# Performance work log

Measured on AMD Instinct MI355X. Metric: run time of the kernel, lower is better.

## Reference

```python
import jax, jax.numpy as jnp
import numpy as np

NUM_HEADS = 32
ROPE_BASE = 10000.0
VISION_TOKEN_TYPE = 1


def _rotate_half(x):
    x1, x2 = jnp.split(x, 2, axis=-1)
    return jnp.concatenate([-x2, x1], axis=-1)


def _rope_cos_sin(position_ids, head_dim, dtype):
    # position_ids: [L] int -> cos/sin [L, head_dim]
    inv_freq = 1.0 / (ROPE_BASE ** (jnp.arange(0, head_dim, 2, dtype=jnp.float32) / head_dim))
    freqs = position_ids.astype(jnp.float32)[:, None] * inv_freq[None, :]  # [L, head_dim//2]
    emb = jnp.concatenate([freqs, freqs], axis=-1)  # [L, head_dim]
    return jnp.cos(emb).astype(dtype), jnp.sin(emb).astype(dtype)


def setup_inputs() -> dict:
    key = jax.random.key(0)
    ks = jax.random.split(key, 7)
    B, L, D = 2, 1024, 4096
    w_scale = 0.02
    return {
        'hidden_states': jax.random.normal(ks[0], (B, L, D), dtype=jnp.float32),
        'token_type_ids': jax.random.randint(ks[1], (B, L), 0, 2, dtype=jnp.int32),
        'position_ids': jnp.arange(L, dtype=jnp.int64),
        'w_qkv_vis': jax.random.normal(ks[2], (D, 3 * D), dtype=jnp.float32) * w_scale,
        'w_qkv_lang': jax.random.normal(ks[3], (D, 3 * D), dtype=jnp.float32) * w_scale,
        'w_dense_vis': jax.random.normal(ks[4], (D, D), dtype=jnp.float32) * w_scale,
        'w_dense_lang': jax.random.normal(ks[5], (D, D), dtype=jnp.float32) * w_scale,
    }


def reference(hidden_states, token_type_ids, position_ids, w_qkv_vis, w_qkv_lang, w_dense_vis, w_dense_lang):
    B, L, D = hidden_states.shape
    H = NUM_HEADS
    Dh = D // H

    # expert masks: a token is 'vision' iff it and the NEXT token are vision type
    tt = token_type_ids
    vmask = jnp.zeros(tt.shape, dtype=bool)
    vmask = vmask.at[:, :-1].set((tt[:, :-1] == VISION_TOKEN_TYPE) & (tt[:, 1:] == VISION_TOKEN_TYPE))  # [B, L]

    # dual-expert fused QKV projection (mask-select between experts)
    qkv = jnp.where(vmask[..., None],
                    hidden_states @ w_qkv_vis,
                    hidden_states @ w_qkv_lang)  # [B, L, 3D]
    q, k, v = jnp.split(qkv, 3, axis=-1)
    q = q.reshape(B, L, H, Dh)
    k = k.reshape(B, L, H, Dh)
    v = v.reshape(B, L, H, Dh)

    # rotary embedding
    cos, sin = _rope_cos_sin(position_ids, Dh, q.dtype)  # [L, Dh]
    cos = cos[None, :, None, :]
    sin = sin[None, :, None, :]
    q = q * cos + _rotate_half(q) * sin
    k = k * cos + _rotate_half(k) * sin

    # causal self-attention (prefill semantics of paged_attention_fwd)
    scale = 1.0 / jnp.sqrt(jnp.asarray(Dh, dtype=q.dtype))
    scores = jnp.einsum('blhd,bmhd->bhlm', q, k) * scale  # [B, H, L, L]
    causal = jnp.tril(jnp.ones((L, L), dtype=bool))
    scores = jnp.where(causal[None, None], scores, jnp.asarray(-1e30, dtype=scores.dtype))
    probs = jax.nn.softmax(scores, axis=-1)
    ctx = jnp.einsum('bhlm,bmhd->blhd', probs, v).reshape(B, L, D)

    # dual-expert output projection
    attn_output = jnp.where(vmask[..., None],
                            ctx @ w_dense_vis,
                            ctx @ w_dense_lang)  # [B, L, D]
    return attn_output
```

## Files before the change

### kernel.cpp

```cpp
#include <hip/hip_runtime.h>
#include <math.h>

typedef unsigned short u16;
typedef __attribute__((ext_vector_type(4))) float f32x4;
typedef __attribute__((ext_vector_type(8))) __bf16 bf16x8;
typedef __attribute__((ext_vector_type(8))) u16 u16x8;
typedef __attribute__((ext_vector_type(4))) u16 u16x4;

#define D_MODEL 4096
#define NQKV    12288
#define BL      2048
#define L_SEQ   1024
#define NH      32
#define DH      128

__device__ __forceinline__ u16 f2bf(float f) {
    union { float f; unsigned u; } v; v.f = f;
    unsigned r = (v.u + 0x7fffu + ((v.u >> 16) & 1u)) >> 16;
    return (u16)r;
}
__device__ __forceinline__ float bf2f(u16 b) {
    union { unsigned u; float f; } v; v.u = ((unsigned)b) << 16;
    return v.f;
}
__device__ __forceinline__ void gload_lds16(const void* g, void* l) {
    __builtin_amdgcn_global_load_lds((const __attribute__((address_space(1))) void*)g,
                                     (__attribute__((address_space(3))) void*)l, 16, 0, 0);
}
__device__ __forceinline__ f32x4 mfma_bf16(bf16x8 a, bf16x8 b, f32x4 c) {
    return __builtin_amdgcn_mfma_f32_16x16x32_bf16(a, b, c, 0, 0, 0);
}

#define BAR()      asm volatile("s_barrier" ::: "memory")
#define WAIT_VM4() asm volatile("s_waitcnt vmcnt(4)" ::: "memory")
#define WAIT_VM0() asm volatile("s_waitcnt vmcnt(0)" ::: "memory")

__global__ __launch_bounds__(256) void convert_f32_bf16(const float* __restrict__ in,
                                                        u16* __restrict__ out, int n4) {
    int i = blockIdx.x * 256 + threadIdx.x;
    if (i < n4) {
        float4 v = ((const float4*)in)[i];
        u16x4 o;
        o[0] = f2bf(v.x); o[1] = f2bf(v.y); o[2] = f2bf(v.z); o[3] = f2bf(v.w);
        ((u16x4*)out)[i] = o;
    }
}

__global__ __launch_bounds__(256) void transpose_convert(const float* __restrict__ W,
                                                         u16* __restrict__ Wt, int K, int N) {
    __shared__ float t[32][33];
    int tx = threadIdx.x, ty = threadIdx.y;
    int nt = blockIdx.x * 32, kt = blockIdx.y * 32;
#pragma unroll
    for (int i = 0; i < 4; ++i)
        t[ty + i * 8][tx] = W[(size_t)(kt + ty + i * 8) * N + nt + tx];
    __syncthreads();
#pragma unroll
    for (int i = 0; i < 4; ++i)
        Wt[(size_t)(nt + ty + i * 8) * K + kt + tx] = f2bf(t[tx][ty + i * 8]);
}

__global__ __launch_bounds__(256) void mask_scan(const int* __restrict__ tt,
                                                 int* __restrict__ lists,
                                                 int* __restrict__ counts) {
    __shared__ int buf[256];
    int tid = threadIdx.x;
    int base = tid * 8;
    int flags = 0, cv = 0;
#pragma unroll
    for (int j = 0; j < 8; ++j) {
        int i = base + j;
        int l = i & (L_SEQ - 1);
        int f = (l < L_SEQ - 1) && (tt[i] == 1) && (tt[i + 1] == 1);
        flags |= f << j; cv += f;
    }
    buf[tid] = cv; __syncthreads();
    for (int d = 1; d < 256; d <<= 1) {
        int t = (tid >= d) ? buf[tid - d] : 0;
        __syncthreads();
        buf[tid] += t;
        __syncthreads();
    }
    int vs = buf[tid] - cv;
    int ls = base - vs;
    int total_v = buf[255];
#pragma unroll
    for (int j = 0; j < 8; ++j) {
        int i = base + j;
        if ((flags >> j) & 1) lists[vs++] = i;
        else                  lists[2048 + ls++] = i;
    }
    if (tid == 0) { counts[0] = total_v; counts[1] = 2048 - total_v; }
}

template <typename OutT>
__global__ __launch_bounds__(512, 2) void gemm_expert(
    const u16* __restrict__ A, const u16* __restrict__ BtVis, const u16* __restrict__ BtLang,
    OutT* __restrict__ C, const int* __restrict__ lists, const int* __restrict__ counts, int ldc) {
    const int e = blockIdx.z;
    const int cnt = counts[e];
    const int m0 = blockIdx.y * 256;
    if (m0 >= cnt) return;
    const u16* Bt = (e == 0) ? BtVis : BtLang;
    const int* list = lists + e * 2048;
    const int n0 = blockIdx.x * 256;
    const int tid = threadIdx.x, lane = tid & 63, w = tid >> 6;
    const int wm = w >> 2, wn = w & 3;
    const int l16 = lane & 15, quad = lane >> 4;

    __shared__ __align__(16) u16 lds[2][2][2][8192];

    const int r0 = tid >> 2;
    const int cs = (tid & 3) ^ ((r0 >> 1) & 3);
    const char* pa0 = (const char*)(A + (size_t)list[min(m0 + r0, cnt - 1)] * D_MODEL) + cs * 16;
    const char* pa1 = (const char*)(A + (size_t)list[min(m0 + 128 + r0, cnt - 1)] * D_MODEL) + cs * 16;
    const char* pb0 = (const char*)(Bt + (size_t)(n0 + r0) * D_MODEL) + cs * 16;
    const char* pb1 = (const char*)(Bt + (size_t)(n0 + 128 + r0) * D_MODEL) + cs * 16;
    const int dst0 = w * 512;
    const int dst1 = 4096 + w * 512;

    auto STAGE = [&](int buf, int mat, int kh, int tk) {
        const int kbyte = tk * 128 + kh * 64;
        const char* g0 = (mat == 0) ? pa0 : pb0;
        const char* g1 = (mat == 0) ? pa1 : pb1;
        u16* d = &lds[buf][mat][kh][0];
        gload_lds16(g0 + kbyte, d + dst0);
        gload_lds16(g1 + kbyte, d + dst1);
    };

    f32x4 acc[8][4] = {};
    const int NT = D_MODEL / 64;

    STAGE(0, 0, 0, 0); STAGE(0, 1, 0, 0); STAGE(0, 0, 1, 0); STAGE(0, 1, 1, 0);
    WAIT_VM4();
    BAR();

    for (int t = 0; t < NT; ++t) {
        const int c = t & 1, nb = c ^ 1;
        const bool pf = (t + 1 < NT);
        bf16x8 af[4], bf[4];

#pragma unroll
        for (int ni = 0; ni < 4; ++ni) {
            int row = wn * 64 + ni * 16 + l16;
            bf[ni] = *(const bf16x8*)&lds[c][1][0][row * 32 + (quad ^ ((row >> 1) & 3)) * 8];
        }
#pragma unroll
        for (int mi = 0; mi < 4; ++mi) {
            int row = wm * 128 + mi * 16 + l16;
            af[mi] = *(const bf16x8*)&lds[c][0][0][row * 32 + (quad ^ ((row >> 1) & 3)) * 8];
        }
        if (pf) STAGE(nb, 0, 0, t + 1);
        BAR();
        __builtin_amdgcn_s_setprio(1);
#pragma unroll
        for (int mi = 0; mi < 4; ++mi)
#pragma unroll
            for (int ni = 0; ni < 4; ++ni)
                acc[mi][ni] = mfma_bf16(af[mi], bf[ni], acc[mi][ni]);
        __builtin_amdgcn_s_setprio(0);
        BAR();

#pragma unroll
        for (int mi = 0; mi < 4; ++mi) {
            int row = wm * 128 + 64 + mi * 16 + l16;
            af[mi] = *(const bf16x8*)&lds[c][0][0][row * 32 + (quad ^ ((row >> 1) & 3)) * 8];
        }
        if (pf) STAGE(nb, 1, 0, t + 1);
        BAR();
        __builtin_amdgcn_s_setprio(1);
#pragma unroll
        for (int mi = 0; mi < 4; ++mi)
#pragma unroll
            for (int ni = 0; ni < 4; ++ni)
                acc[4 + mi][ni] = mfma_bf16(af[mi], bf[ni], acc[4 + mi][ni]);
        __builtin_amdgcn_s_setprio(0);
        if (pf) WAIT_VM4(); else WAIT_VM0();
        BAR();

#pragma unroll
        for (int ni = 0; ni < 4; ++ni) {
            int row = wn * 64 + ni * 16 + l16;
            bf[ni] = *(const bf16x8*)&lds[c][1][1][row * 32 + (quad ^ ((row >> 1) & 3)) * 8];
        }
#pragma unroll
        for (int mi = 0; mi < 4; ++mi) {
            int row = wm * 128 + mi * 16 + l16;
            af[mi] = *(const bf16x8*)&lds[c][0][1][row * 32 + (quad ^ ((row >> 1) & 3)) * 8];
        }
        if (pf) STAGE(nb, 0, 1, t + 1);
        BAR();
        __builtin_amdgcn_s_setprio(1);
#pragma unroll
        for (int mi = 0; mi < 4; ++mi)
#pragma unroll
            for (int ni = 0; ni < 4; ++ni)
                acc[mi][ni] = mfma_bf16(af[mi], bf[ni], acc[mi][ni]);
        __builtin_amdgcn_s_setprio(0);
        BAR();

#pragma unroll
        for (int mi = 0; mi < 4; ++mi) {
            int row = wm * 128 + 64 + mi * 16 + l16;
            af[mi] = *(const bf16x8*)&lds[c][0][1][row * 32 + (quad ^ ((row >> 1) & 3)) * 8];
        }
        if (pf) STAGE(nb, 1, 1, t + 1);
        BAR();
        __builtin_amdgcn_s_setprio(1);
#pragma unroll
        for (int mi = 0; mi < 4; ++mi)
#pragma unroll
            for (int ni = 0; ni < 4; ++ni)
                acc[4 + mi][ni] = mfma_bf16(af[mi], bf[ni], acc[4 + mi][ni]);
        __builtin_amdgcn_s_setprio(0);
        if (pf) WAIT_VM4();
        BAR();
    }

#pragma unroll
    for (int mf = 0; mf < 8; ++mf) {
#pragma unroll
        for (int r = 0; r < 4; ++r) {
            int slot = m0 + wm * 128 + mf * 16 + quad * 4 + r;
            if (slot < cnt) {
                int row = list[slot];
                size_t rb = (size_t)row * ldc + n0 + wn * 64 + l16;
#pragma unroll
                for (int ni = 0; ni < 4; ++ni) {
                    float v = acc[mf][ni][r];
                    if constexpr (sizeof(OutT) == 2) C[rb + ni * 16] = (OutT)f2bf(v);
                    else                             C[rb + ni * 16] = v;
                }
            }
        }
    }
}

__global__ __launch_bounds__(256) void rope_kernel(u16* __restrict__ qkv,
                                                   const int* __restrict__ posi) {
    int idx = blockIdx.x * 256 + threadIdx.x;
    int t = idx >> 11;
    int rem = idx & 2047;
    int h = rem >> 6;
    int j = rem & 63;
    int l = t & (L_SEQ - 1);
    int is_i32 = posi[1];
    int pv = is_i32 ? posi[l] : posi[2 * l];
    float p = (float)pv;
    float inv = expf(-(float)j * 0.14391156831212787f);
    float ang = p * inv;
    float s, c;
    sincosf(ang, &s, &c);
    size_t base = (size_t)t * NQKV + h * DH + j;
    float x1 = bf2f(qkv[base]), x2 = bf2f(qkv[base + 64]);
    qkv[base]      = f2bf(x1 * c - x2 * s);
    qkv[base + 64] = f2bf(x2 * c + x1 * s);
    size_t kb = base + D_MODEL;
    x1 = bf2f(qkv[kb]); x2 = bf2f(qkv[kb + 64]);
    qkv[kb]      = f2bf(x1 * c - x2 * s);
    qkv[kb + 64] = f2bf(x2 * c + x1 * s);
}

__global__ __launch_bounds__(256, 2) void attn_kernel(const u16* __restrict__ qkv,
                                                      u16* __restrict__ ctx) {
    const int qt = (int)gridDim.x - 1 - (int)blockIdx.x;
    const int h = blockIdx.y, b = blockIdx.z;
    const int tid = threadIdx.x, lane = tid & 63, w = tid >> 6;
    const int quad = lane >> 4, l16 = lane & 15;

    __shared__ __align__(16) u16 Ks[2][64 * 128];
    __shared__ __align__(16) u16 Vt[2][128 * 64];
    __shared__ __align__(16) u16 Ps[4][16 * 64];

    const size_t qbase = ((size_t)(b * L_SEQ + qt * 64 + w * 16 + l16)) * NQKV + h * DH;
    bf16x8 aq[4];
#pragma unroll
    for (int kc = 0; kc < 4; ++kc)
        aq[kc] = *(const bf16x8*)&qkv[qbase + kc * 32 + quad * 8];

    int srow[4], schk[4];
#pragma unroll
    for (int i = 0; i < 4; ++i) {
        int idx = i * 256 + tid;
        srow[i] = idx >> 4;
        schk[i] = idx & 15;
    }
    const size_t kv0 = ((size_t)(b * L_SEQ)) * NQKV + D_MODEL + h * DH;

    float m_i[4], l_i[4];
    f32x4 o[8] = {};
#pragma unroll
    for (int r = 0; r < 4; ++r) { m_i[r] = -1e30f; l_i[r] = 0.f; }
    const float scale = 0.08838834764831845f;
    const int jmax = qt + 1;

    {
        u16x8 kr[4], vr[4];
#pragma unroll
        for (int i = 0; i < 4; ++i) {
            size_t g = kv0 + (size_t)srow[i] * NQKV + schk[i] * 8;
            kr[i] = *(const u16x8*)&qkv[g];
            vr[i] = *(const u16x8*)&qkv[g + D_MODEL];
        }
#pragma unroll
        for (int i = 0; i < 4; ++i) {
            int r = srow[i], c = schk[i];
            *(u16x8*)&Ks[0][r * 128 + ((c ^ (r & 7)) * 8)] = kr[i];
#pragma unroll
            for (int e = 0; e < 8; ++e) {
                int d = c * 8 + e;
                int sw = (r >> 3) ^ ((d ^ (d >> 3)) & 7);
                Vt[0][d * 64 + sw * 8 + (r & 7)] = vr[i][e];
            }
        }
    }
    __syncthreads();

    for (int jt = 0; jt < jmax; ++jt) {
        const int cur = jt & 1;
        const bool pf = (jt + 1 < jmax);

        u16x8 kr[4], vr[4];
        if (pf) {
            const size_t kb = kv0 + (size_t)((jt + 1) * 64) * NQKV;
#pragma unroll
            for (int i = 0; i < 4; ++i) {
                size_t g = kb + (size_t)srow[i] * NQKV + schk[i] * 8;
                kr[i] = *(const u16x8*)&qkv[g];
                vr[i] = *(const u16x8*)&qkv[g + D_MODEL];
            }
        }

        f32x4 s[4] = {};
        __builtin_amdgcn_s_setprio(1);
#pragma unroll
        for (int sub = 0; sub < 4; ++sub) {
            const int row = sub * 16 + l16;
#pragma unroll
            for (int kc = 0; kc < 4; ++kc) {
                bf16x8 bk = *(const bf16x8*)&Ks[cur][row * 128 + (((kc * 4 + quad) ^ (row & 7)) * 8)];
                s[sub] = mfma_bf16(aq[kc], bk, s[sub]);
            }
        }
        __builtin_amdgcn_s_setprio(0);

        const int qg = qt * 64 + w * 16 + quad * 4;
        float p[4][4], mx[4];
#pragma unroll
        for (int r = 0; r < 4; ++r) mx[r] = -1e30f;
#pragma unroll
        for (int sub = 0; sub < 4; ++sub) {
            const int kg = jt * 64 + sub * 16 + l16;
#pragma unroll
            for (int r = 0; r < 4; ++r) {
                float sv = (kg <= qg + r) ? s[sub][r] * scale : -1e30f;
                p[sub][r] = sv;
                mx[r] = fmaxf(mx[r], sv);
            }
        }
#pragma unroll
        for (int d = 1; d < 16; d <<= 1)
#pragma unroll
            for (int r = 0; r < 4; ++r) mx[r] = fmaxf(mx[r], __shfl_xor(mx[r], d));
        float alpha[4], rs[4];
#pragma unroll
        for (int r = 0; r < 4; ++r) {
            float mn = fmaxf(m_i[r], mx[r]);
            alpha[r] = __expf(m_i[r] - mn);
            m_i[r] = mn;
            rs[r] = 0.f;
        }
#pragma unroll
        for (int sub = 0; sub < 4; ++sub)
#pragma unroll
            for (int r = 0; r < 4; ++r) {
                p[sub][r] = __expf(p[sub][r] - m_i[r]);
                rs[r] += p[sub][r];
            }
#pragma unroll
        for (int d = 1; d < 16; d <<= 1)
#pragma unroll
            for (int r = 0; r < 4; ++r) rs[r] += __shfl_xor(rs[r], d);

#pragma unroll
        for (int sub = 0; sub < 4; ++sub)
#pragma unroll
            for (int r = 0; r < 4; ++r) {
                const int q = quad * 4 + r;
                const int chunk = sub * 2 + (l16 >> 3);
                Ps[w][q * 64 + ((chunk ^ (q & 7)) * 8) + (l16 & 7)] = f2bf(p[sub][r]);
            }
#pragma unroll
        for (int r = 0; r < 4; ++r) l_i[r] = l_i[r] * alpha[r] + rs[r];
#pragma unroll
        for (int n = 0; n < 8; ++n)
#pragma unroll
            for (int r = 0; r < 4; ++r) o[n][r] *= alpha[r];

        __builtin_amdgcn_s_setprio(1);
#pragma unroll
        for (int ks = 0; ks < 2; ++ks) {
            bf16x8 ap = *(const bf16x8*)&Ps[w][l16 * 64 + (((ks * 4 + quad) ^ (l16 & 7)) * 8)];
#pragma unroll
            for (int n = 0; n < 8; ++n) {
                const int d = n * 16 + l16;
                bf16x8 bv = *(const bf16x8*)&Vt[cur][d * 64 + (((ks * 4 + quad) ^ ((d ^ (d >> 3)) & 7)) * 8)];
                o[n] = mfma_bf16(ap, bv, o[n]);
            }
        }
        __builtin_amdgcn_s_setprio(0);

        if (pf) {
            const int nb = cur ^ 1;
#pragma unroll
            for (int i = 0; i < 4; ++i) {
                int r = srow[i], c = schk[i];
                *(u16x8*)&Ks[nb][r * 128 + ((c ^ (r & 7)) * 8)] = kr[i];
#pragma unroll
                for (int e = 0; e < 8; ++e) {
                    int d = c * 8 + e;
                    int sw = (r >> 3) ^ ((d ^ (d >> 3)) & 7);
                    Vt[nb][d * 64 + sw * 8 + (r & 7)] = vr[i][e];
                }
            }
        }
        __syncthreads();
    }

    const int tglob = b * L_SEQ + qt * 64 + w * 16 + quad * 4;
#pragma unroll
    for (int r = 0; r < 4; ++r) {
        float invl = 1.f / l_i[r];
#pragma unroll
        for (int n = 0; n < 8; ++n)
            ctx[(size_t)(tglob + r) * D_MODEL + h * DH + n * 16 + l16] = f2bf(o[n][r] * invl);
    }
}

extern "C" void kernel_launch(void* const* d_in, const int* in_sizes, int n_in,
                              void* d_out, int out_size, void* d_ws, size_t ws_size,
                              hipStream_t stream) {
    const float* hidden = (const float*)d_in[0];
    const int* tt = (const int*)d_in[1];
    const int* pos = (const int*)d_in[2];
    const float* wqv = (const float*)d_in[3];
    const float* wql = (const float*)d_in[4];
    const float* wdv = (const float*)d_in[5];
    const float* wdl = (const float*)d_in[6];
    float* out = (float*)d_out;

    char* ws = (char*)d_ws;
    size_t off = 0;
    auto alloc = [&](size_t bytes) {
        char* p = ws + off;
        off += (bytes + 255) & ~(size_t)255;
        return p;
    };
    u16* WqvT = (u16*)alloc((size_t)NQKV * D_MODEL * 2);
    u16* WqlT = (u16*)alloc((size_t)NQKV * D_MODEL * 2);
    u16* WdvT = (u16*)alloc((size_t)D_MODEL * D_MODEL * 2);
    u16* WdlT = (u16*)alloc((size_t)D_MODEL * D_MODEL * 2);
    u16* Abf  = (u16*)alloc((size_t)BL * D_MODEL * 2);
    u16* QKV  = (u16*)alloc((size_t)BL * NQKV * 2);
    u16* CTX  = (u16*)alloc((size_t)BL * D_MODEL * 2);
    int* lists  = (int*)alloc(4096 * sizeof(int));
    int* counts = (int*)alloc(256);

    convert_f32_bf16<<<BL * D_MODEL / 4 / 256, 256, 0, stream>>>(hidden, Abf, BL * D_MODEL / 4);
    transpose_convert<<<dim3(NQKV / 32, D_MODEL / 32), dim3(32, 8), 0, stream>>>(wqv, WqvT, D_MODEL, NQKV);
    transpose_convert<<<dim3(NQKV / 32, D_MODEL / 32), dim3(32, 8), 0, stream>>>(wql, WqlT, D_MODEL, NQKV);
    transpose_convert<<<dim3(D_MODEL / 32, D_MODEL / 32), dim3(32, 8), 0, stream>>>(wdv, WdvT, D_MODEL, D_MODEL);
    transpose_convert<<<dim3(D_MODEL / 32, D_MODEL / 32), dim3(32, 8), 0, stream>>>(wdl, WdlT, D_MODEL, D_MODEL);
    mask_scan<<<1, 256, 0, stream>>>(tt, lists, counts);
    gemm_expert<u16><<<dim3(NQKV / 256, 8, 2), 512, 0, stream>>>(Abf, WqvT, WqlT, QKV, lists, counts, NQKV);
    rope_kernel<<<BL * NH * 64 / 256, 256, 0, stream>>>(QKV, pos);
    attn_kernel<<<dim3(16, NH, 2), 256, 0, stream>>>(QKV, CTX);
    gemm_expert<float><<<dim3(D_MODEL / 256, 8, 2), 512, 0, stream>>>(CTX, WdvT, WdlT, out, lists, counts, D_MODEL);
}
```

Measured before the change: 1.025 ms.

## Use 5-slot LDS ring in expert GEMM, rewrite weight transpose, fast rope math

The expert GEMM swaps its double-buffered 4-quarter LDS layout for a 5-slot ring. Each quarter-tile load is issued right after the MFMA block that frees a slot, so prefetch runs deeper, and launch bounds rise to 4 blocks per SM. The weight transpose-convert drops the shared-memory tile: each thread now reads 8 strided floats and writes one 16-byte packed bf16 vector. RoPE uses the fast __expf/__sincosf intrinsics. Risks include lower accuracy in RoPE, strided uncoalesced global reads in the transpose, and register pressure from the higher occupancy target with 128 accumulators.

```diff
diff --git a/kernel.cpp b/kernel.cpp
--- a/kernel.cpp
+++ b/kernel.cpp
@@ -48,16 +48,14 @@
 
 __global__ __launch_bounds__(256) void transpose_convert(const float* __restrict__ W,
                                                          u16* __restrict__ Wt, int K, int N) {
-    __shared__ float t[32][33];
-    int tx = threadIdx.x, ty = threadIdx.y;
-    int nt = blockIdx.x * 32, kt = blockIdx.y * 32;
-#pragma unroll
-    for (int i = 0; i < 4; ++i)
-        t[ty + i * 8][tx] = W[(size_t)(kt + ty + i * 8) * N + nt + tx];
-    __syncthreads();
-#pragma unroll
-    for (int i = 0; i < 4; ++i)
-        Wt[(size_t)(nt + ty + i * 8) * K + kt + tx] = f2bf(t[tx][ty + i * 8]);
+    const int l = threadIdx.x & 63, w = threadIdx.x >> 6;
+    const int nt = blockIdx.x * 64, kt = blockIdx.y * 32 + w * 8;
+    const int n = nt + l;
+    u16x8 o;
+#pragma unroll
+    for (int j = 0; j < 8; ++j)
+        o[j] = f2bf(W[(size_t)(kt + j) * N + n]);
+    *(u16x8*)&Wt[(size_t)n * K + kt] = o;
 }
 
 __global__ __launch_bounds__(256) void mask_scan(const int* __restrict__ tt,
@@ -94,7 +92,7 @@
 }
 
 template <typename OutT>
-__global__ __launch_bounds__(512, 2) void gemm_expert(
+__global__ __launch_bounds__(512, 4) void gemm_expert(
     const u16* __restrict__ A, const u16* __restrict__ BtVis, const u16* __restrict__ BtLang,
     OutT* __restrict__ C, const int* __restrict__ lists, const int* __restrict__ counts, int ldc) {
     const int e = blockIdx.z;
@@ -108,7 +106,7 @@
     const int wm = w >> 2, wn = w & 3;
     const int l16 = lane & 15, quad = lane >> 4;
 
-    __shared__ __align__(16) u16 lds[2][2][2][8192];
+    __shared__ __align__(16) u16 ring[5][8192];
 
     const int r0 = tid >> 2;
     const int cs = (tid & 3) ^ ((r0 >> 1) & 3);
@@ -119,11 +117,11 @@
     const int dst0 = w * 512;
     const int dst1 = 4096 + w * 512;
 
-    auto STAGE = [&](int buf, int mat, int kh, int tk) {
-        const int kbyte = tk * 128 + kh * 64;
-        const char* g0 = (mat == 0) ? pa0 : pb0;
-        const char* g1 = (mat == 0) ? pa1 : pb1;
-        u16* d = &lds[buf][mat][kh][0];
+    auto STAGE = [&](int slot, int u4, int tk) {
+        const int kbyte = tk * 128 + ((u4 & 2) ? 64 : 0);
+        const char* g0 = (u4 & 1) ? pb0 : pa0;
+        const char* g1 = (u4 & 1) ? pb1 : pa1;
+        u16* d = &ring[slot][0];
         gload_lds16(g0 + kbyte, d + dst0);
         gload_lds16(g1 + kbyte, d + dst1);
     };
@@ -131,26 +129,28 @@
     f32x4 acc[8][4] = {};
     const int NT = D_MODEL / 64;
 
-    STAGE(0, 0, 0, 0); STAGE(0, 1, 0, 0); STAGE(0, 0, 1, 0); STAGE(0, 1, 1, 0);
+    STAGE(0, 0, 0); STAGE(1, 1, 0); STAGE(2, 2, 0); STAGE(3, 3, 0);
     WAIT_VM4();
     BAR();
 
+    int sA = 0;
+    int ss = 4;
+    int us = 4;
+
     for (int t = 0; t < NT; ++t) {
-        const int c = t & 1, nb = c ^ 1;
-        const bool pf = (t + 1 < NT);
+        const int s0 = sA, s1 = (sA + 1) % 5, s2 = (sA + 2) % 5, s3 = (sA + 3) % 5;
         bf16x8 af[4], bf[4];
 
 #pragma unroll
         for (int ni = 0; ni < 4; ++ni) {
             int row = wn * 64 + ni * 16 + l16;
-            bf[ni] = *(const bf16x8*)&lds[c][1][0][row * 32 + (quad ^ ((row >> 1) & 3)) * 8];
+            bf[ni] = *(const bf16x8*)&ring[s1][row * 32 + (quad ^ ((row >> 1) & 3)) * 8];
         }
 #pragma unroll
         for (int mi = 0; mi < 4; ++mi) {
             int row = wm * 128 + mi * 16 + l16;
-            af[mi] = *(const bf16x8*)&lds[c][0][0][row * 32 + (quad ^ ((row >> 1) & 3)) * 8];
-        }
-        if (pf) STAGE(nb, 0, 0, t + 1);
+            af[mi] = *(const bf16x8*)&ring[s0][row * 32 + (quad ^ ((row >> 1) & 3)) * 8];
+        }
         BAR();
         __builtin_amdgcn_s_setprio(1);
 #pragma unroll
@@ -160,13 +160,13 @@
                 acc[mi][ni] = mfma_bf16(af[mi], bf[ni], acc[mi][ni]);
         __builtin_amdgcn_s_setprio(0);
         BAR();
+        if (us < 4 * NT) { STAGE(ss, us & 3, us >> 2); ss = (ss + 1) % 5; ++us; }
 
 #pragma unroll
         for (int mi = 0; mi < 4; ++mi) {
             int row = wm * 128 + 64 + mi * 16 + l16;
-            af[mi] = *(const bf16x8*)&lds[c][0][0][row * 32 + (quad ^ ((row >> 1) & 3)) * 8];
-        }
-        if (pf) STAGE(nb, 1, 0, t + 1);
+            af[mi] = *(const bf16x8*)&ring[s0][row * 32 + (quad ^ ((row >> 1) & 3)) * 8];
+        }
         BAR();
         __builtin_amdgcn_s_setprio(1);
 #pragma unroll
@@ -175,20 +175,21 @@
             for (int ni = 0; ni < 4; ++ni)
                 acc[4 + mi][ni] = mfma_bf16(af[mi], bf[ni], acc[4 + mi][ni]);
         __builtin_amdgcn_s_setprio(0);
-        if (pf) WAIT_VM4(); else WAIT_VM0();
+        BAR();
+        if (us < 4 * NT) { STAGE(ss, us & 3, us >> 2); ss = (ss + 1) % 5; ++us; }
+        if (t == NT - 1) WAIT_VM0(); else WAIT_VM4();
         BAR();
 
 #pragma unroll
         for (int ni = 0; ni < 4; ++ni) {
             int row = wn * 64 + ni * 16 + l16;
-            bf[ni] = *(const bf16x8*)&lds[c][1][1][row * 32 + (quad ^ ((row >> 1) & 3)) * 8];
+            bf[ni] = *(const bf16x8*)&ring[s3][row * 32 + (quad ^ ((row >> 1) & 3)) * 8];
         }
 #pragma unroll
         for (int mi = 0; mi < 4; ++mi) {
             int row = wm * 128 + mi * 16 + l16;
-            af[mi] = *(const bf16x8*)&lds[c][0][1][row * 32 + (quad ^ ((row >> 1) & 3)) * 8];
-        }
-        if (pf) STAGE(nb, 0, 1, t + 1);
+            af[mi] = *(const bf16x8*)&ring[s2][row * 32 + (quad ^ ((row >> 1) & 3)) * 8];
+        }
         BAR();
         __builtin_amdgcn_s_setprio(1);
 #pragma unroll
@@ -198,13 +199,13 @@
                 acc[mi][ni] = mfma_bf16(af[mi], bf[ni], acc[mi][ni]);
         __builtin_amdgcn_s_setprio(0);
         BAR();
+        if (us < 4 * NT) { STAGE(ss, us & 3, us >> 2); ss = (ss + 1) % 5; ++us; }
 
 #pragma unroll
         for (int mi = 0; mi < 4; ++mi) {
             int row = wm * 128 + 64 + mi * 16 + l16;
-            af[mi] = *(const bf16x8*)&lds[c][0][1][row * 32 + (quad ^ ((row >> 1) & 3)) * 8];
-        }
-        if (pf) STAGE(nb, 1, 1, t + 1);
+            af[mi] = *(const bf16x8*)&ring[s2][row * 32 + (quad ^ ((row >> 1) & 3)) * 8];
+        }
         BAR();
         __builtin_amdgcn_s_setprio(1);
 #pragma unroll
@@ -213,8 +214,11 @@
             for (int ni = 0; ni < 4; ++ni)
                 acc[4 + mi][ni] = mfma_bf16(af[mi], bf[ni], acc[4 + mi][ni]);
         __builtin_amdgcn_s_setprio(0);
-        if (pf) WAIT_VM4();
-        BAR();
+        BAR();
+        if (us < 4 * NT) { STAGE(ss, us & 3, us >> 2); ss = (ss + 1) % 5; ++us; }
+        if (t + 1 < NT) { WAIT_VM4(); BAR(); }
+
+        sA = (sA + 4) % 5;
     }
 
 #pragma unroll
@@ -247,10 +251,10 @@
     int is_i32 = posi[1];
     int pv = is_i32 ? posi[l] : posi[2 * l];
     float p = (float)pv;
-    float inv = expf(-(float)j * 0.14391156831212787f);
+    float inv = __expf(-(float)j * 0.14391156831212787f);
     float ang = p * inv;
     float s, c;
-    sincosf(ang, &s, &c);
+    __sincosf(ang, &s, &c);
     size_t base = (size_t)t * NQKV + h * DH + j;
     float x1 = bf2f(qkv[base]), x2 = bf2f(qkv[base + 64]);
     qkv[base]      = f2bf(x1 * c - x2 * s);
@@ -467,10 +471,10 @@
     int* counts = (int*)alloc(256);
 
     convert_f32_bf16<<<BL * D_MODEL / 4 / 256, 256, 0, stream>>>(hidden, Abf, BL * D_MODEL / 4);
-    transpose_convert<<<dim3(NQKV / 32, D_MODEL / 32), dim3(32, 8), 0, stream>>>(wqv, WqvT, D_MODEL, NQKV);
-    transpose_convert<<<dim3(NQKV / 32, D_MODEL / 32), dim3(32, 8), 0, stream>>>(wql, WqlT, D_MODEL, NQKV);
-    transpose_convert<<<dim3(D_MODEL / 32, D_MODEL / 32), dim3(32, 8), 0, stream>>>(wdv, WdvT, D_MODEL, D_MODEL);
-    transpose_convert<<<dim3(D_MODEL / 32, D_MODEL / 32), dim3(32, 8), 0, stream>>>(wdl, WdlT, D_MODEL, D_MODEL);
+    transpose_convert<<<dim3(NQKV / 64, D_MODEL / 32), 256, 0, stream>>>(wqv, WqvT, D_MODEL, NQKV);
+    transpose_convert<<<dim3(NQKV / 64, D_MODEL / 32), 256, 0, stream>>>(wql, WqlT, D_MODEL, NQKV);
+    transpose_convert<<<dim3(D_MODEL / 64, D_MODEL / 32), 256, 0, stream>>>(wdv, WdvT, D_MODEL, D_MODEL);
+    transpose_convert<<<dim3(D_MODEL / 64, D_MODEL / 32), 256, 0, stream>>>(wdl, WdlT, D_MODEL, D_MODEL);
     mask_scan<<<1, 256, 0, stream>>>(tt, lists, counts);
     gemm_expert<u16><<<dim3(NQKV / 256, 8, 2), 512, 0, stream>>>(Abf, WqvT, WqlT, QKV, lists, counts, NQKV);
     rope_kernel<<<BL * NH * 64 / 256, 256, 0, stream>>>(QKV, pos);
```

Result: slower. 3.991 ms (+289.2%).
